# Kernel tuning notes

Hardware: AMD Instinct MI355X
Metric: run time of the kernel (lower is better)

## Reference

```python
import jax, jax.numpy as jnp
import numpy as np

B, L, D, H = 2, 2048, 1024, 16


def setup_inputs() -> dict:
    key = jax.random.key(0)
    ks = jax.random.split(key, 6)
    return {
        "x": jax.random.normal(ks[0], (B, L, D), dtype=jnp.float32),
        "w_qkv": jax.random.normal(ks[1], (3 * D, D), dtype=jnp.float32) * (D ** -0.5),
        "b_qkv": jax.random.normal(ks[2], (3 * D,), dtype=jnp.float32) * 0.02,
        "w_out": jax.random.normal(ks[3], (D, D), dtype=jnp.float32) * (D ** -0.5),
        "b_out": jax.random.normal(ks[4], (D,), dtype=jnp.float32) * 0.02,
        "lam": jnp.float32(0.5),
        "heads": H,
    }


def reference(x, w_qkv, b_qkv, w_out, b_out, lam, heads):
    b, l, d = x.shape
    dh = d // heads
    scale = d ** -0.5  # NOTE: module scales by d_model**-0.5, not head_dim**-0.5

    qkv = x @ w_qkv.T + b_qkv                      # [B, L, 3D]
    qkv = qkv.reshape(b, l, 3, heads, dh)
    qkv = jnp.transpose(qkv, (2, 0, 3, 1, 4))      # [3, B, H, L, dh]
    q, k, v = qkv[0], qkv[1], qkv[2]

    k_prev = jnp.roll(k, shift=1, axis=2)          # roll along sequence dim

    s_cur = jnp.einsum("bhqd,bhkd->bhqk", q, k) * scale
    s_prev = jnp.einsum("bhqd,bhkd->bhqk", q, k_prev) * scale

    a1 = jax.nn.softmax(s_cur, axis=-1)
    a2 = jax.nn.softmax(s_prev, axis=-1)
    diff = lam * (a1 - a2)                         # dropout = identity (eval)

    o = jnp.einsum("bhqk,bhkd->bhqd", diff, v)     # [B, H, L, dh]
    o = jnp.transpose(o, (0, 2, 1, 3)).reshape(b, l, d)
    return o @ w_out.T + b_out
```

## Files before the change

### kernel.cpp

```cpp
#include <hip/hip_runtime.h>
#include <hip/hip_bf16.h>
#include <stdint.h>


typedef __attribute__((ext_vector_type(8))) short s16x8;
typedef __attribute__((ext_vector_type(4))) short s16x4;
typedef __attribute__((ext_vector_type(4))) float f32x4;
typedef __attribute__((ext_vector_type(4))) unsigned int u32x4;

__device__ __forceinline__ float bf2f(unsigned short u) {
    union { unsigned int i; float f; } x; x.i = ((unsigned int)u) << 16; return x.f;
}
__device__ __forceinline__ unsigned short f2bf(float f) {
    union { float f; unsigned int i; } x; x.f = f;
    unsigned int r = x.i + 0x7FFFu + ((x.i >> 16) & 1u);
    return (unsigned short)(r >> 16);
}

__device__ __forceinline__ void gload16(const void* g, void* l) {
    auto gp = reinterpret_cast<const __attribute__((address_space(1))) unsigned int*>(
        reinterpret_cast<uintptr_t>(g));
    auto lp = reinterpret_cast<__attribute__((address_space(3))) unsigned int*>(
        reinterpret_cast<uintptr_t>(l));
    __builtin_amdgcn_global_load_lds(gp, lp, 16, 0, 0);
}

__global__ __launch_bounds__(256) void cvt_all(
    const float* __restrict__ x, const float* __restrict__ wq,
    const float* __restrict__ wo,
    unsigned short* __restrict__ xb, unsigned short* __restrict__ wqb,
    unsigned short* __restrict__ wob)
{
    int i4 = blockIdx.x * 256 + threadIdx.x;
    const float* src; unsigned short* dst; int off;
    if (i4 < 1048576)            { src = x;  dst = xb;  off = i4; }
    else if (i4 < 1048576 + 786432) { src = wq; dst = wqb; off = i4 - 1048576; }
    else                         { src = wo; dst = wob; off = i4 - 1835008; }
    float4 v = ((const float4*)src)[off];
    ushort4 u;
    u.x = f2bf(v.x); u.y = f2bf(v.y); u.z = f2bf(v.z); u.w = f2bf(v.w);
    ((ushort4*)dst)[off] = u;
}

__global__ __launch_bounds__(256) void vd_transpose(
    const unsigned short* __restrict__ qkvb, unsigned short* __restrict__ vdt)
{
    __shared__ unsigned short T[64][72];
    const int tid = threadIdx.x;
    const int j0 = blockIdx.x * 64;
    const int bh = blockIdx.y, b = bh >> 4, h = bh & 15;
    const unsigned short* vb = qkvb + (size_t)b * 2048 * 3072 + 2048 + h * 64;

    int r = tid >> 2, cq = tid & 3;
    int rp = (r & 35) | ((r & 12) << 1) | ((r & 16) >> 2);
    int j = j0 + r, jn = (j + 1) & 2047;
    const unsigned short* p0 = vb + (size_t)j  * 3072 + cq * 16;
    const unsigned short* p1 = vb + (size_t)jn * 3072 + cq * 16;
    s16x8 a0 = *(const s16x8*)p0, a1 = *(const s16x8*)(p0 + 8);
    s16x8 b0 = *(const s16x8*)p1, b1 = *(const s16x8*)(p1 + 8);
#pragma unroll
    for (int u = 0; u < 8; ++u)
        T[cq * 16 + u][rp] = f2bf(bf2f((unsigned short)a0[u]) - bf2f((unsigned short)b0[u]));
#pragma unroll
    for (int u = 0; u < 8; ++u)
        T[cq * 16 + 8 + u][rp] = f2bf(bf2f((unsigned short)a1[u]) - bf2f((unsigned short)b1[u]));
    __syncthreads();

    int row = tid >> 2, sc = tid & 3;
    s16x8 o0 = *(const s16x8*)&T[row][sc * 16];
    s16x8 o1 = *(const s16x8*)&T[row][sc * 16 + 8];
    unsigned short* dst = vdt + ((size_t)bh * 64 + row) * 2048 + j0 + sc * 16;
    *(s16x8*)dst = o0;
    *(s16x8*)(dst + 8) = o1;
}

template <int OUT_BF16, int BN>
__global__ __launch_bounds__(256) void gemm_nt_mfma(
    const unsigned short* __restrict__ A,
    const unsigned short* __restrict__ Bm,
    const float* __restrict__ bias,
    void* __restrict__ C,
    int M, int N, int K, int nscale, float smul)
{
    constexpr int NT = BN / 32;
    __shared__ unsigned short As[2][128][32];
    __shared__ unsigned short Bs[2][BN][32];

    const int tid = threadIdx.x;
    const int wave = tid >> 6, lane = tid & 63;
    const int quad = lane >> 4, ln = lane & 15;
    const int wm = (wave >> 1) * 64, wn = (wave & 1) * (NT * 16);
    const int m0 = blockIdx.y * 128, n0 = blockIdx.x * BN;
    const int rA = wave * 16 + (lane >> 2);
    const int gsl = lane & 3;

    f32x4 acc[4][NT];
#pragma unroll
    for (int mt = 0; mt < 4; ++mt)
#pragma unroll
        for (int nt = 0; nt < NT; ++nt) acc[mt][nt] = f32x4{0.f, 0.f, 0.f, 0.f};

    auto stage = [&](int p, int k0) {
#pragma unroll
        for (int q = 0; q < 2; ++q) {
            int row = q * 64 + rA;
            int kg = gsl ^ ((row >> 1) & 3);
            gload16(A + (size_t)(m0 + row) * K + k0 + kg * 8,
                    &As[p][q * 64 + wave * 16][0]);
            if (q * 64 < BN)
                gload16(Bm + (size_t)(n0 + row) * K + k0 + kg * 8,
                        &Bs[p][q * 64 + wave * 16][0]);
        }
    };

    stage(0, 0);
    __syncthreads();
    int p = 0;
    for (int k0 = 0; k0 < K; k0 += 32) {
        if (k0 + 32 < K) stage(p ^ 1, k0 + 32);
        s16x8 af[4], bfr[NT];
#pragma unroll
        for (int mt = 0; mt < 4; ++mt) {
            int rr = wm + mt * 16 + ln;
            af[mt] = *(const s16x8*)&As[p][rr][((quad ^ ((rr >> 1) & 3)) & 3) * 8];
        }
#pragma unroll
        for (int nt = 0; nt < NT; ++nt) {
            int rr = wn + nt * 16 + ln;
            bfr[nt] = *(const s16x8*)&Bs[p][rr][((quad ^ ((rr >> 1) & 3)) & 3) * 8];
        }
#pragma unroll
        for (int mt = 0; mt < 4; ++mt)
#pragma unroll
            for (int nt = 0; nt < NT; ++nt)
                acc[mt][nt] = __builtin_amdgcn_mfma_f32_16x16x32_bf16(
                    af[mt], bfr[nt], acc[mt][nt], 0, 0, 0);
        __syncthreads();
        p ^= 1;
    }

    float bb[NT];
#pragma unroll
    for (int nt = 0; nt < NT; ++nt) bb[nt] = bias[n0 + wn + nt * 16 + ln];
#pragma unroll
    for (int mt = 0; mt < 4; ++mt)
#pragma unroll
        for (int nt = 0; nt < NT; ++nt) {
            int col = n0 + wn + nt * 16 + ln;
            float sc = (col < nscale) ? smul : 1.f;
#pragma unroll
            for (int rg = 0; rg < 4; ++rg) {
                int row = m0 + wm + mt * 16 + quad * 4 + rg;
                float v = (acc[mt][nt][rg] + bb[nt]) * sc;
                if (OUT_BF16)
                    ((unsigned short*)C)[(size_t)row * N + col] = f2bf(v);
                else
                    ((float*)C)[(size_t)row * N + col] = v;
            }
        }
}

__global__ __launch_bounds__(512) void diff_attn_v9(
    const unsigned short* __restrict__ qkv,
    const unsigned short* __restrict__ vdt,
    const float* __restrict__ lam_p,
    unsigned short* __restrict__ o_ws)
{
    constexpr int L = 2048, TD = 3072;

    __shared__ __align__(16) unsigned char smem[65536];
    auto Ks = reinterpret_cast<unsigned short(*)[64][64]>(smem);
    auto Vs = reinterpret_cast<unsigned short(*)[64][64]>(smem + 32768);
    auto Red = reinterpret_cast<f32x4(*)[2][4][64]>(smem);
    auto Lred = reinterpret_cast<float(*)[2][64]>(smem + 32768);

    const int tid = threadIdx.x;
    const int wave = tid >> 6, lane = tid & 63;
    const int qw = wave & 3, jw = wave >> 2;
    const int quad = lane >> 4, ln = lane & 15;
    const int bh = blockIdx.y, b = bh >> 4, h = bh & 15;
    const int q0 = blockIdx.x * 128;
    const size_t seqbase = (size_t)b * L;
    const unsigned short* base = qkv + seqbase * TD + h * 64;
    const unsigned short* kb = base + 1024;
    const unsigned short* vbase = vdt + (size_t)bh * 64 * 2048;

    const int lsl = lane >> 3;
    const int cgl = (lane & 7) ^ lsl;

    const float lam = lam_p[0];
    asm volatile("" :: "v"(lam));

    s16x8 qf[2][2];
#pragma unroll
    for (int s = 0; s < 2; ++s) {
        const unsigned short* qrow =
            base + (size_t)(q0 + qw * 32 + s * 16 + ln) * TD;
        qf[s][0] = *(const s16x8*)(qrow + quad * 8);
        qf[s][1] = *(const s16x8*)(qrow + 32 + quad * 8);
    }

    auto stage = [&](int p, int j0) {
        const unsigned short* k0p = kb + (size_t)(j0 + wave * 8 + lsl) * TD + cgl * 8;
        gload16(k0p, &Ks[p][wave * 8][0]);
        const unsigned short* v0p = vbase + (size_t)(wave * 8 + lsl) * 2048 + j0 + cgl * 8;
        gload16(v0p, &Vs[p][wave * 8][0]);
    };

    f32x4 Ot[2][4];
    f32x4 lacc[2];
#pragma unroll
    for (int s = 0; s < 2; ++s) {
        lacc[s] = f32x4{0.f, 0.f, 0.f, 0.f};
#pragma unroll
        for (int mt = 0; mt < 4; ++mt) Ot[s][mt] = f32x4{0.f, 0.f, 0.f, 0.f};
    }

    const s16x8 ones8 = {(short)0x3F80, (short)0x3F80, (short)0x3F80, (short)0x3F80,
                         (short)0x3F80, (short)0x3F80, (short)0x3F80, (short)0x3F80};
    const int kx0 = (quad ^ (ln & 7)) << 3;
    const int kx1 = ((quad + 4) ^ (ln & 7)) << 3;
    const int vx  = (((jw * 4 + quad) ^ (ln & 7))) << 3;

    stage(0, 0);
    stage(1, 64);
    asm volatile("s_waitcnt vmcnt(0)" ::: "memory");
    __builtin_amdgcn_s_barrier();
    asm volatile("" ::: "memory");

    for (int i = 0; i < 16; ++i) {
        const int pb = (i & 1) * 2;

        if (i + 1 < 16) {
            stage(pb ^ 2, (2 * i + 2) * 64);
            stage((pb ^ 2) + 1, (2 * i + 3) * 64);
        }

#pragma unroll
        for (int u = 0; u < 2; ++u) {
            const int c = pb + u;

            f32x4 ST[2][2];
#pragma unroll
            for (int t = 0; t < 2; ++t) {
                const int t2 = jw * 2 + t;
                s16x8 k0 = *(const s16x8*)&Ks[c][t2 * 16 + ln][kx0];
                s16x8 k1 = *(const s16x8*)&Ks[c][t2 * 16 + ln][kx1];
#pragma unroll
                for (int s = 0; s < 2; ++s) {
                    f32x4 z = f32x4{0.f, 0.f, 0.f, 0.f};
                    z = __builtin_amdgcn_mfma_f32_16x16x32_bf16(k0, qf[s][0], z, 0, 0, 0);
                    z = __builtin_amdgcn_mfma_f32_16x16x32_bf16(k1, qf[s][1], z, 0, 0, 0);
                    ST[s][t] = z;
                }
            }

            s16x8 pf8[2];
#pragma unroll
            for (int s = 0; s < 2; ++s) {
                unsigned int w[4];
#pragma unroll
                for (int t = 0; t < 2; ++t) {
                    unsigned int b0 = __builtin_bit_cast(unsigned int,
                        __builtin_amdgcn_exp2f(ST[s][t][0]));
                    unsigned int b1 = __builtin_bit_cast(unsigned int,
                        __builtin_amdgcn_exp2f(ST[s][t][1]));
                    unsigned int b2 = __builtin_bit_cast(unsigned int,
                        __builtin_amdgcn_exp2f(ST[s][t][2]));
                    unsigned int b3 = __builtin_bit_cast(unsigned int,
                        __builtin_amdgcn_exp2f(ST[s][t][3]));
                    w[t * 2]     = (b0 >> 16) | (b1 & 0xFFFF0000u);
                    w[t * 2 + 1] = (b2 >> 16) | (b3 & 0xFFFF0000u);
                }
                pf8[s] = __builtin_bit_cast(s16x8, (u32x4){w[0], w[1], w[2], w[3]});
            }

#pragma unroll
            for (int s = 0; s < 2; ++s)
                lacc[s] = __builtin_amdgcn_mfma_f32_16x16x32_bf16(
                    ones8, pf8[s], lacc[s], 0, 0, 0);

#pragma unroll
            for (int mt = 0; mt < 4; ++mt) {
                s16x8 vf = *(const s16x8*)&Vs[c][mt * 16 + ln][vx];
#pragma unroll
                for (int s = 0; s < 2; ++s)
                    Ot[s][mt] = __builtin_amdgcn_mfma_f32_16x16x32_bf16(
                        vf, pf8[s], Ot[s][mt], 0, 0, 0);
            }
        }

        asm volatile("s_waitcnt vmcnt(0)" ::: "memory");
        __builtin_amdgcn_s_barrier();
        asm volatile("" ::: "memory");
    }

    if (jw == 1) {
#pragma unroll
        for (int s = 0; s < 2; ++s) {
            Lred[qw][s][lane] = lacc[s][0];
#pragma unroll
            for (int mt = 0; mt < 4; ++mt) Red[qw][s][mt][lane] = Ot[s][mt];
        }
    }
    __syncthreads();
    if (jw == 0) {
#pragma unroll
        for (int s = 0; s < 2; ++s) {
            float lsum = lacc[s][0] + Lred[qw][s][lane];
            float inv = lam / lsum;
            int row = q0 + qw * 32 + s * 16 + ln;
            unsigned short* orow = o_ws + (seqbase + row) * 1024 + h * 64 + quad * 4;
#pragma unroll
            for (int mt = 0; mt < 4; ++mt) {
                f32x4 r = Red[qw][s][mt][lane];
                ushort4 u;
                u.x = f2bf((Ot[s][mt][0] + r[0]) * inv);
                u.y = f2bf((Ot[s][mt][1] + r[1]) * inv);
                u.z = f2bf((Ot[s][mt][2] + r[2]) * inv);
                u.w = f2bf((Ot[s][mt][3] + r[3]) * inv);
                *(ushort4*)(orow + mt * 16) = u;
            }
        }
    }
}

extern "C" void kernel_launch(void* const* d_in, const int* in_sizes, int n_in,
                              void* d_out, int out_size, void* d_ws, size_t ws_size,
                              hipStream_t stream) {
    const float* x     = (const float*)d_in[0];
    const float* w_qkv = (const float*)d_in[1];
    const float* b_qkv = (const float*)d_in[2];
    const float* w_out = (const float*)d_in[3];
    const float* b_out = (const float*)d_in[4];
    const float* lam   = (const float*)d_in[5];
    float* out = (float*)d_out;

    unsigned short* xb   = (unsigned short*)d_ws;
    unsigned short* wqb  = xb   + (size_t)4096 * 1024;
    unsigned short* wob  = wqb  + (size_t)3072 * 1024;
    unsigned short* qkvb = wob  + (size_t)1024 * 1024;
    unsigned short* ob   = qkvb + (size_t)4096 * 3072;
    unsigned short* vdt  = ob   + (size_t)4096 * 1024;

    cvt_all<<<8192, 256, 0, stream>>>(x, w_qkv, w_out, xb, wqb, wob);

    gemm_nt_mfma<1, 128><<<dim3(24, 32), 256, 0, stream>>>(
        xb, wqb, b_qkv, qkvb, 4096, 3072, 1024, 1024, 0.045084222f);

    vd_transpose<<<dim3(32, 32), 256, 0, stream>>>(qkvb, vdt);

    diff_attn_v9<<<dim3(16, 32), 512, 0, stream>>>(qkvb, vdt, lam, ob);

    gemm_nt_mfma<0, 64><<<dim3(16, 32), 256, 0, stream>>>(
        ob, wob, b_out, out, 4096, 1024, 1024, 0, 1.f);
}
```

Before: 186.2 us.

## Pipeline attention K/V staging per tile with finer waits and MFMA priority

Restructures the attention main loop so each 64-key tile issues its own async global-to-LDS load two tiles ahead and then waits with vmcnt(2) instead of draining all loads every two tiles. This gives a rolling four-buffer pipeline with a barrier per tile. It also raises wave priority around the MFMA sections and replaces manual truncating bf16 packing with the hardware v_cvt_pk_bf16_f32 instruction, which rounds instead of truncating. The trailing loads wrap around with redundant prefetches, and there are more barriers per key tile.

```diff
diff --git a/kernel.cpp b/kernel.cpp
--- a/kernel.cpp
+++ b/kernel.cpp
@@ -15,6 +15,12 @@
     union { float f; unsigned int i; } x; x.f = f;
     unsigned int r = x.i + 0x7FFFu + ((x.i >> 16) & 1u);
     return (unsigned short)(r >> 16);
+}
+
+__device__ __forceinline__ unsigned int cvtpk(float lo, float hi) {
+    unsigned int r;
+    asm("v_cvt_pk_bf16_f32 %0, %1, %2" : "=v"(r) : "v"(lo), "v"(hi));
+    return r;
 }
 
 __device__ __forceinline__ void gload16(const void* g, void* l) {
@@ -160,7 +166,7 @@
         }
 }
 
-__global__ __launch_bounds__(512) void diff_attn_v9(
+__global__ __launch_bounds__(512) void diff_attn_v10(
     const unsigned short* __restrict__ qkv,
     const unsigned short* __restrict__ vdt,
     const float* __restrict__ lam_p,
@@ -200,12 +206,8 @@
         qf[s][1] = *(const s16x8*)(qrow + 32 + quad * 8);
     }
 
-    auto stage = [&](int p, int j0) {
-        const unsigned short* k0p = kb + (size_t)(j0 + wave * 8 + lsl) * TD + cgl * 8;
-        gload16(k0p, &Ks[p][wave * 8][0]);
-        const unsigned short* v0p = vbase + (size_t)(wave * 8 + lsl) * 2048 + j0 + cgl * 8;
-        gload16(v0p, &Vs[p][wave * 8][0]);
-    };
+    const unsigned short* kstage = kb + (size_t)(wave * 8 + lsl) * TD + cgl * 8;
+    const unsigned short* vstage = vbase + (size_t)(wave * 8 + lsl) * 2048 + cgl * 8;
 
     f32x4 Ot[2][4];
     f32x4 lacc[2];
@@ -222,78 +224,87 @@
     const int kx1 = ((quad + 4) ^ (ln & 7)) << 3;
     const int vx  = (((jw * 4 + quad) ^ (ln & 7))) << 3;
 
-    stage(0, 0);
-    stage(1, 64);
-    asm volatile("s_waitcnt vmcnt(0)" ::: "memory");
+    auto body = [&](auto cc, auto ccs, int j0s) {
+        constexpr int c  = decltype(cc)::value;
+        constexpr int cs = decltype(ccs)::value;
+
+        gload16(kstage + (size_t)j0s * TD, &Ks[cs][wave * 8][0]);
+        gload16(vstage + j0s,              &Vs[cs][wave * 8][0]);
+
+        f32x4 ST[2][2];
+        __builtin_amdgcn_s_setprio(1);
+#pragma unroll
+        for (int t = 0; t < 2; ++t) {
+            const int t2 = jw * 2 + t;
+            s16x8 k0 = *(const s16x8*)&Ks[c][t2 * 16 + ln][kx0];
+            s16x8 k1 = *(const s16x8*)&Ks[c][t2 * 16 + ln][kx1];
+#pragma unroll
+            for (int s = 0; s < 2; ++s) {
+                f32x4 z = f32x4{0.f, 0.f, 0.f, 0.f};
+                z = __builtin_amdgcn_mfma_f32_16x16x32_bf16(k0, qf[s][0], z, 0, 0, 0);
+                z = __builtin_amdgcn_mfma_f32_16x16x32_bf16(k1, qf[s][1], z, 0, 0, 0);
+                ST[s][t] = z;
+            }
+        }
+        __builtin_amdgcn_s_setprio(0);
+
+        s16x8 pf8[2];
+#pragma unroll
+        for (int s = 0; s < 2; ++s) {
+            unsigned int w[4];
+#pragma unroll
+            for (int t = 0; t < 2; ++t) {
+                float e0 = __builtin_amdgcn_exp2f(ST[s][t][0]);
+                float e1 = __builtin_amdgcn_exp2f(ST[s][t][1]);
+                float e2 = __builtin_amdgcn_exp2f(ST[s][t][2]);
+                float e3 = __builtin_amdgcn_exp2f(ST[s][t][3]);
+                w[t * 2]     = cvtpk(e0, e1);
+                w[t * 2 + 1] = cvtpk(e2, e3);
+            }
+            pf8[s] = __builtin_bit_cast(s16x8, (u32x4){w[0], w[1], w[2], w[3]});
+        }
+
+        __builtin_amdgcn_s_setprio(1);
+#pragma unroll
+        for (int s = 0; s < 2; ++s)
+            lacc[s] = __builtin_amdgcn_mfma_f32_16x16x32_bf16(
+                ones8, pf8[s], lacc[s], 0, 0, 0);
+#pragma unroll
+        for (int mt = 0; mt < 4; ++mt) {
+            s16x8 vf = *(const s16x8*)&Vs[c][mt * 16 + ln][vx];
+#pragma unroll
+            for (int s = 0; s < 2; ++s)
+                Ot[s][mt] = __builtin_amdgcn_mfma_f32_16x16x32_bf16(
+                    vf, pf8[s], Ot[s][mt], 0, 0, 0);
+        }
+        __builtin_amdgcn_s_setprio(0);
+
+        asm volatile("s_waitcnt vmcnt(2)" ::: "memory");
+        __builtin_amdgcn_s_barrier();
+        asm volatile("" ::: "memory");
+    };
+
+    gload16(kstage, &Ks[0][wave * 8][0]);
+    gload16(vstage, &Vs[0][wave * 8][0]);
+    gload16(kstage + (size_t)64 * TD, &Ks[1][wave * 8][0]);
+    gload16(vstage + 64,              &Vs[1][wave * 8][0]);
+    asm volatile("s_waitcnt vmcnt(2)" ::: "memory");
     __builtin_amdgcn_s_barrier();
     asm volatile("" ::: "memory");
 
-    for (int i = 0; i < 16; ++i) {
-        const int pb = (i & 1) * 2;
-
-        if (i + 1 < 16) {
-            stage(pb ^ 2, (2 * i + 2) * 64);
-            stage((pb ^ 2) + 1, (2 * i + 3) * 64);
-        }
-
-#pragma unroll
-        for (int u = 0; u < 2; ++u) {
-            const int c = pb + u;
-
-            f32x4 ST[2][2];
-#pragma unroll
-            for (int t = 0; t < 2; ++t) {
-                const int t2 = jw * 2 + t;
-                s16x8 k0 = *(const s16x8*)&Ks[c][t2 * 16 + ln][kx0];
-                s16x8 k1 = *(const s16x8*)&Ks[c][t2 * 16 + ln][kx1];
-#pragma unroll
-                for (int s = 0; s < 2; ++s) {
-                    f32x4 z = f32x4{0.f, 0.f, 0.f, 0.f};
-                    z = __builtin_amdgcn_mfma_f32_16x16x32_bf16(k0, qf[s][0], z, 0, 0, 0);
-                    z = __builtin_amdgcn_mfma_f32_16x16x32_bf16(k1, qf[s][1], z, 0, 0, 0);
-                    ST[s][t] = z;
-                }
-            }
-
-            s16x8 pf8[2];
-#pragma unroll
-            for (int s = 0; s < 2; ++s) {
-                unsigned int w[4];
-#pragma unroll
-                for (int t = 0; t < 2; ++t) {
-                    unsigned int b0 = __builtin_bit_cast(unsigned int,
-                        __builtin_amdgcn_exp2f(ST[s][t][0]));
-                    unsigned int b1 = __builtin_bit_cast(unsigned int,
-                        __builtin_amdgcn_exp2f(ST[s][t][1]));
-                    unsigned int b2 = __builtin_bit_cast(unsigned int,
-                        __builtin_amdgcn_exp2f(ST[s][t][2]));
-                    unsigned int b3 = __builtin_bit_cast(unsigned int,
-                        __builtin_amdgcn_exp2f(ST[s][t][3]));
-                    w[t * 2]     = (b0 >> 16) | (b1 & 0xFFFF0000u);
-                    w[t * 2 + 1] = (b2 >> 16) | (b3 & 0xFFFF0000u);
-                }
-                pf8[s] = __builtin_bit_cast(s16x8, (u32x4){w[0], w[1], w[2], w[3]});
-            }
-
-#pragma unroll
-            for (int s = 0; s < 2; ++s)
-                lacc[s] = __builtin_amdgcn_mfma_f32_16x16x32_bf16(
-                    ones8, pf8[s], lacc[s], 0, 0, 0);
-
-#pragma unroll
-            for (int mt = 0; mt < 4; ++mt) {
-                s16x8 vf = *(const s16x8*)&Vs[c][mt * 16 + ln][vx];
-#pragma unroll
-                for (int s = 0; s < 2; ++s)
-                    Ot[s][mt] = __builtin_amdgcn_mfma_f32_16x16x32_bf16(
-                        vf, pf8[s], Ot[s][mt], 0, 0, 0);
-            }
-        }
-
-        asm volatile("s_waitcnt vmcnt(0)" ::: "memory");
-        __builtin_amdgcn_s_barrier();
-        asm volatile("" ::: "memory");
-    }
+    using I0 = std::integral_constant<int, 0>;
+    using I1 = std::integral_constant<int, 1>;
+    using I2 = std::integral_constant<int, 2>;
+    using I3 = std::integral_constant<int, 3>;
+    for (int it = 0; it < 8; ++it) {
+        const int kt4 = it * 4;
+        body(I0{}, I2{}, ((kt4 + 2) & 31) * 64);
+        body(I1{}, I3{}, ((kt4 + 3) & 31) * 64);
+        body(I2{}, I0{}, ((kt4 + 4) & 31) * 64);
+        body(I3{}, I1{}, ((kt4 + 5) & 31) * 64);
+    }
+
+    __syncthreads();
 
     if (jw == 1) {
 #pragma unroll
@@ -350,7 +361,7 @@
 
     vd_transpose<<<dim3(32, 32), 256, 0, stream>>>(qkvb, vdt);
 
-    diff_attn_v9<<<dim3(16, 32), 512, 0, stream>>>(qkvb, vdt, lam, ob);
+    diff_attn_v10<<<dim3(16, 32), 512, 0, stream>>>(qkvb, vdt, lam, ob);
 
     gemm_nt_mfma<0, 64><<<dim3(16, 32), 256, 0, stream>>>(
         ob, wob, b_out, out, 4096, 1024, 1024, 0, 1.f);
```

After: 184.5 us. No clear change (-0.9%).
